# Kernel optimization log

Measured on AMD Instinct MI355X. Metric: run time of the kernel, lower is better.

Reference implementation:

```python
import jax, jax.numpy as jnp
import numpy as np

H = 256      # input_size == hidden_size
N = 512      # x dim0: acts as LSTM time axis (torch unbatched 2D LSTM input)
S = 128      # x dim1: independent seq positions (outer python loop in torch)
UP = 4       # upscale


def setup_inputs() -> dict:
    key = jax.random.key(0)
    ks = jax.random.split(key, 9)
    k_init = 1.0 / np.sqrt(H)
    u = lambda k, shape: jax.random.uniform(k, shape, jnp.float32, -k_init, k_init)
    return {
        "x": jax.random.normal(ks[0], (N, S, H), jnp.float32),
        # PyTorch nn.LSTM params, gate order (i, f, g, o)
        "Wih0": u(ks[1], (4 * H, H)), "Whh0": u(ks[2], (4 * H, H)),
        "bih0": u(ks[3], (4 * H,)),   "bhh0": u(ks[4], (4 * H,)),
        "Wih1": u(ks[5], (4 * H, H)), "Whh1": u(ks[6], (4 * H, H)),
        "bih1": u(ks[7], (4 * H,)),   "bhh1": u(ks[8], (4 * H,)),
    }


def _lstm_layer(x, h0, c0, Wih, Whh, b):
    """Scan one LSTM layer over the time axis. x: [N, S, H], h0/c0: [S, H]."""
    def step(carry, xt):
        h, c = carry
        g = xt @ Wih.T + h @ Whh.T + b            # [S, 4H]
        i, f, gg, o = jnp.split(g, 4, axis=-1)
        i = jax.nn.sigmoid(i)
        f = jax.nn.sigmoid(f)
        gg = jnp.tanh(gg)
        o = jax.nn.sigmoid(o)
        c = f * c + i * gg
        h = o * jnp.tanh(c)
        return (h, c), h
    (hT, cT), ys = jax.lax.scan(step, (h0, c0), x)
    return ys, hT, cT


def reference(x, Wih0, Whh0, bih0, bhh0, Wih1, Whh1, bih1, bhh1):
    n, s, hdim = x.shape
    # state per seq position (torch's outer loop is vectorized as batch S)
    h = jnp.zeros((2, s, hdim), x.dtype)
    c = jnp.zeros((2, s, hdim), x.dtype)
    b0 = bih0 + bhh0
    b1 = bih1 + bhh1
    data = [x]
    cur = x
    for _ in range(UP - 1):
        y0, h0n, c0n = _lstm_layer(cur, h[0], c[0], Wih0, Whh0, b0)
        y1, h1n, c1n = _lstm_layer(y0, h[1], c[1], Wih1, Whh1, b1)
        h = jnp.stack([h0n, h1n])
        c = jnp.stack([c0n, c1n])
        cur = y1
        data.append(y1)
    # torch interleaves per seq position: [..., s*UP + k, ...] = data[k][:, s, :]
    out = jnp.stack(data, axis=2)          # [N, S, UP, H]
    return out.reshape(n, s * UP, hdim)
```

## Files before the change

### kernel.cpp

```cpp
#include <hip/hip_runtime.h>
#include <stdint.h>

#define Hh 256
#define Sd 128
#define Nt 512
#define NPASS 3
#define TSTEPS (NPASS*Nt)
#define RBLK 16
#define POIS 0x7F80u
#define LEAD 192

typedef float f32x4 __attribute__((ext_vector_type(4)));
typedef __bf16 bf16x8 __attribute__((ext_vector_type(8)));
typedef unsigned short u16x8 __attribute__((ext_vector_type(8)));
typedef unsigned long long ull;
typedef ull ull2 __attribute__((ext_vector_type(2)));

#define HBUF_ELEMS ((size_t)Nt*Sd*Hh)
#define WPACK_OFF  (2ull*HBUF_ELEMS*2)
#define FLAGS_OFF  (WPACK_OFF + 2097152ull)

__device__ __forceinline__ unsigned short f2bf(float f) {
  unsigned u = __builtin_bit_cast(unsigned, f);
  u += 0x7FFFu + ((u >> 16) & 1u);
  return (unsigned short)(u >> 16);
}
__device__ __forceinline__ ull pk4(float a, float b, float c, float d) {
  return (ull)f2bf(a) | ((ull)f2bf(b) << 16) | ((ull)f2bf(c) << 32) | ((ull)f2bf(d) << 48);
}
__device__ __forceinline__ bool hasPois(ull v) {
  return ((unsigned short)(v)       == (unsigned short)POIS) |
         ((unsigned short)(v >> 16) == (unsigned short)POIS) |
         ((unsigned short)(v >> 32) == (unsigned short)POIS) |
         ((unsigned short)(v >> 48) == (unsigned short)POIS);
}
__device__ __forceinline__ ull ld8(const void* p) {
  return __hip_atomic_load((ull*)p, __ATOMIC_RELAXED, __HIP_MEMORY_SCOPE_AGENT);
}
__device__ __forceinline__ void st8c(void* p, ull v) {
  __hip_atomic_store((ull*)p, v, __ATOMIC_RELAXED, __HIP_MEMORY_SCOPE_AGENT);
}
__device__ __forceinline__ void poll2(const ull* p, ull& a0, ull& a1) {
  while (hasPois(a0) | hasPois(a1)) {
    __builtin_amdgcn_s_sleep(1);
    if (hasPois(a0)) a0 = ld8(p);
    if (hasPois(a1)) a1 = ld8(p + 1);
  }
}
__device__ __forceinline__ void bar_lgkm() {
  __builtin_amdgcn_sched_barrier(0);
  asm volatile("s_waitcnt lgkmcnt(0)" ::: "memory");
  __builtin_amdgcn_s_barrier();
  __builtin_amdgcn_sched_barrier(0);
}

__global__ void pack_w(const float* __restrict__ Wih0, const float* __restrict__ Whh0,
                       const float* __restrict__ Wih1, const float* __restrict__ Whh1,
                       unsigned short* __restrict__ wpack) {
  int id = blockIdx.x * 256 + threadIdx.x;
  int ln = id & 63;
  int kt = (id >> 6) & 15;
  int w  = (id >> 10) & 7;
  int g2 = (id >> 13) & 7;
  int l  = (id >> 16) & 1;
  int col = (w >> 1)*256 + g2*32 + (w & 1)*16 + (ln & 15);
  int k0 = kt*32 + (ln >> 4)*8;
  const float* Wih = l ? Wih1 : Wih0;
  const float* Whh = l ? Whh1 : Whh0;
  const float* src = (k0 < 256) ? (Wih + (size_t)col*256 + k0)
                                : (Whh + (size_t)col*256 + (k0 - 256));
  u16x8 v;
#pragma unroll
  for (int j = 0; j < 8; ++j) v[j] = f2bf(src[j]);
  *(u16x8*)(wpack + (size_t)id * 8) = v;
}

__global__ void copy_x(const float* __restrict__ x, float* __restrict__ out) {
  int id = blockIdx.x * 256 + threadIdx.x;
  int n  = id >> 13;
  int s  = (id >> 6) & 127;
  int h4 = id & 63;
  const float4 v = *(const float4*)(x + ((size_t)n*Sd + s)*Hh + h4*4);
  *(float4*)(out + ((size_t)n*(Sd*4) + s*4)*Hh + h4*4) = v;
}

__global__ void poison_hbuf(unsigned int* __restrict__ p) {
  size_t i = (size_t)blockIdx.x * 256 + threadIdx.x;
  uint4 v = make_uint4(0x7F807F80u, 0x7F807F80u, 0x7F807F80u, 0x7F807F80u);
  *(uint4*)(p + i*4) = v;
}

__global__ void __launch_bounds__(512) lstm_persist(
    const float* __restrict__ x,
    const float* __restrict__ bih0, const float* __restrict__ bhh0,
    const float* __restrict__ bih1, const float* __restrict__ bhh1,
    const unsigned short* __restrict__ wpack,
    unsigned short* __restrict__ hbuf,
    unsigned int* __restrict__ prog,
    float* __restrict__ out)
{
  const int b = blockIdx.x;
  const int r = b & 7;
  const int g2 = (b >> 3) & 7;
  const int l = (b >> 6) & 1;
  const int tid = threadIdx.x;
  const int ln = tid & 63;
  const int w  = tid >> 6;

  __shared__ __align__(16) unsigned short AinB[2][RBLK * 256];
  __shared__ __align__(16) unsigned short Ah[RBLK * 256];
  __shared__ float gates[RBLK][132];

  bf16x8 B[16];
  {
    const unsigned short* base = wpack + ((size_t)((l*8 + g2)*8 + w)) * 8192 + (size_t)ln * 8;
#pragma unroll
    for (int kt = 0; kt < 16; ++kt) {
      u16x8 u = *(const u16x8*)(base + kt * 512);
      B[kt] = __builtin_bit_cast(bf16x8, u);
    }
  }

  const int srow = tid >> 5;
  const int cc   = tid & 31;
  const int s    = r*RBLK + srow;
  const int hcol = g2*32 + cc;
  float bias[4];
  {
    const float* bi = l ? bih1 : bih0;
    const float* bh = l ? bhh1 : bhh0;
#pragma unroll
    for (int q = 0; q < 4; ++q) {
      int col = q*256 + g2*32 + cc;
      bias[q] = bi[col] + bh[col];
    }
  }
  float cst = 0.f;

  const int row_f = ln & 15;
  const int kg16  = (ln >> 4) * 16;
  const int swr   = (row_f & 7) << 4;
  const int stAddr = srow*512 + ((cc*16) ^ ((srow & 7) << 4));

  unsigned int* flagL1 = prog + r*8;
  unsigned int* myFlag = prog + r*8 + g2;
  const unsigned short* hbufL0 = hbuf;
  unsigned short* hbufSelf = hbuf + (size_t)l * HBUF_ELEMS;

  float4 pxa, pxb;
  ull pa = 0, pb = 0;
  ull hpa = 0, hpb = 0;

  auto writeAin = [&](int buf, ull lo, ull hi) {
    ull2 v = {lo, hi};
    *(ull2*)((char*)AinB[buf] + stAddr) = v;
  };
  auto prefetchAin = [&](int T2) {
    const int t2 = T2 & 511, p2 = T2 >> 9;
    if (l == 1) {
      const ull* ip = (const ull*)(hbufL0 + ((size_t)t2*Sd + s)*Hh + cc*8);
      pa = ld8(ip); pb = ld8(ip + 1);
    } else if (p2 == 0) {
      const float* xb = x + ((size_t)t2*Sd + s)*Hh + cc*8;
      pxa = *(const float4*)(xb);
      pxb = *(const float4*)(xb + 4);
    } else {
      const float* ob = out + ((size_t)t2*(Sd*4) + s*4 + p2)*Hh + cc*8;
      pxa = *(const float4*)(ob);
      pxb = *(const float4*)(ob + 4);
    }
  };
  auto consumeAin = [&](int T1) {
    const int buf = T1 & 1;
    if (l == 1) {
      if (hasPois(pa) | hasPois(pb)) {
        const int t1 = T1 & 511;
        const ull* ip = (const ull*)(hbufL0 + ((size_t)t1*Sd + s)*Hh + cc*8);
        poll2(ip, pa, pb);
      }
      writeAin(buf, pa, pb);
    } else {
      writeAin(buf, pk4(pxa.x, pxa.y, pxa.z, pxa.w), pk4(pxb.x, pxb.y, pxb.z, pxb.w));
    }
  };

#define MFMA4(BUF, BOFF)                                                            \
  {                                                                                 \
    _Pragma("unroll")                                                               \
    for (int kt = 0; kt < 8; kt += 2) {                                             \
      int off0 = row_f*512 + (( kt     *64 + kg16) ^ swr);                          \
      int off1 = row_f*512 + (((kt + 1)*64 + kg16) ^ swr);                          \
      u16x8 a0 = *(const u16x8*)((const char*)(BUF) + off0);                        \
      u16x8 a1 = *(const u16x8*)((const char*)(BUF) + off1);                        \
      acc0 = __builtin_amdgcn_mfma_f32_16x16x32_bf16(                               \
               __builtin_bit_cast(bf16x8, a0), B[BOFF + kt],     acc0, 0,0,0);      \
      acc1 = __builtin_amdgcn_mfma_f32_16x16x32_bf16(                               \
               __builtin_bit_cast(bf16x8, a1), B[BOFF + kt + 1], acc1, 0,0,0);      \
    }                                                                               \
  }

  f32x4 acc0 = {0.f,0.f,0.f,0.f}, acc1 = {0.f,0.f,0.f,0.f};
  if (l == 1) {
    const ull* ip = (const ull*)(hbufL0 + (size_t)s*Hh + cc*8);
    ull a0 = ld8(ip), a1 = ld8(ip + 1);
    poll2(ip, a0, a1);
    writeAin(0, a0, a1);
  } else {
    const float* xb = x + (size_t)s*Hh + cc*8;
    float4 v0 = *(const float4*)(xb), v1 = *(const float4*)(xb + 4);
    writeAin(0, pk4(v0.x, v0.y, v0.z, v0.w), pk4(v1.x, v1.y, v1.z, v1.w));
  }
  prefetchAin(1);
  __syncthreads();
  MFMA4(AinB[0], 0)

  for (int T = 0; T < TSTEPS; ++T) {
    const int p = T >> 9;
    const int t = T & 511;

    if (T > 0) {
      const ull* ap = (const ull*)(hbufSelf + ((size_t)((T - 1) & 511)*Sd + s)*Hh + cc*8);
      ull a0 = hpa, a1 = hpb;
      while (hasPois(a0) | hasPois(a1)) {
        if (hasPois(a0)) a0 = ld8(ap);
        if (hasPois(a1)) a1 = ld8(ap + 1);
      }
      ull2 v2 = {a0, a1};
      *(ull2*)((char*)Ah + stAddr) = v2;
    } else {
      ull2 v2 = {0ull, 0ull};
      *(ull2*)((char*)Ah + stAddr) = v2;
    }
    if (T + 1 < TSTEPS) consumeAin(T + 1);
    if (l == 0 && (T & 15) == 0 && tid < 8) {
      int need = T - LEAD;
      if (need > 0)
        while ((int)__hip_atomic_load(flagL1 + tid, __ATOMIC_RELAXED, __HIP_MEMORY_SCOPE_AGENT) < need)
          __builtin_amdgcn_s_sleep(1);
    }
    bar_lgkm();

    if (T > 0) MFMA4(Ah, 8)

    {
      const int colb = (w >> 1)*32 + (w & 1)*16 + (ln & 15);
      const int rowb = (ln >> 4)*4;
#pragma unroll
      for (int j = 0; j < 4; ++j)
        gates[rowb + j][colb] = acc0[j] + acc1[j];
    }
    bar_lgkm();

    {
      float G0 = gates[srow][cc]      + bias[0];
      float G1 = gates[srow][32 + cc] + bias[1];
      float G2 = gates[srow][64 + cc] + bias[2];
      float G3 = gates[srow][96 + cc] + bias[3];
      float gi = 1.f/(1.f + __expf(-G0));
      float gf = 1.f/(1.f + __expf(-G1));
      float gg = 1.f - 2.f/(1.f + __expf(2.f*G2));
      float go = 1.f/(1.f + __expf(-G3));
      cst = gf*cst + gi*gg;
      float th = 1.f - 2.f/(1.f + __expf(2.f*cst));
      float hv = go*th;
      float h1 = __shfl_down(hv, 1);
      float h2 = __shfl_down(hv, 2);
      float h3 = __shfl_down(hv, 3);
      if ((cc & 3) == 0) {
        st8c(hbufSelf + ((size_t)t*Sd + s)*Hh + hcol, pk4(hv, h1, h2, h3));
        st8c(hbufSelf + ((size_t)((T + 256) & 511)*Sd + s)*Hh + hcol,
             0x7F807F807F807F80ull);
      }
      if (l == 1 && (cc & 1) == 0) {
        ull o01 = ((ull)__builtin_bit_cast(unsigned, hv))
                | ((ull)__builtin_bit_cast(unsigned, h1) << 32);
        st8c(out + ((size_t)t*(Sd*4) + s*4 + (p + 1))*Hh + hcol, o01);
      }
    }
    if (l == 1 && (T & 15) == 15 && tid == 0)
      __hip_atomic_store(myFlag, (unsigned)(T + 1), __ATOMIC_RELAXED, __HIP_MEMORY_SCOPE_AGENT);
    if (T + 2 < TSTEPS) prefetchAin(T + 2);
    if (T + 1 < TSTEPS) {
      const ull* ap = (const ull*)(hbufSelf + ((size_t)(T & 511)*Sd + s)*Hh + cc*8);
      hpa = ld8(ap);
      hpb = ld8(ap + 1);
    }
    acc0 = (f32x4){0.f,0.f,0.f,0.f};
    acc1 = (f32x4){0.f,0.f,0.f,0.f};
    if (T + 1 < TSTEPS) MFMA4(AinB[(T + 1) & 1], 0)
  }
}

extern "C" void kernel_launch(void* const* d_in, const int* in_sizes, int n_in,
                              void* d_out, int out_size, void* d_ws, size_t ws_size,
                              hipStream_t stream) {
  const float* x    = (const float*)d_in[0];
  const float* Wih0 = (const float*)d_in[1];
  const float* Whh0 = (const float*)d_in[2];
  const float* bih0 = (const float*)d_in[3];
  const float* bhh0 = (const float*)d_in[4];
  const float* Wih1 = (const float*)d_in[5];
  const float* Whh1 = (const float*)d_in[6];
  const float* bih1 = (const float*)d_in[7];
  const float* bhh1 = (const float*)d_in[8];
  float* out = (float*)d_out;
  char* ws = (char*)d_ws;

  if (ws_size < FLAGS_OFF + 4096) return;

  unsigned short* hbuf  = (unsigned short*)ws;
  unsigned short* wpack = (unsigned short*)(ws + WPACK_OFF);
  unsigned int*   prog  = (unsigned int*)(ws + FLAGS_OFF);

  (void)hipMemsetAsync(prog, 0, 1024, stream);
  hipLaunchKernelGGL(poison_hbuf, dim3(16384), dim3(256), 0, stream, (unsigned int*)hbuf);
  hipLaunchKernelGGL(pack_w, dim3(512), dim3(256), 0, stream, Wih0, Whh0, Wih1, Whh1, wpack);
  hipLaunchKernelGGL(copy_x, dim3(16384), dim3(256), 0, stream, x, out);
  hipLaunchKernelGGL(lstm_persist, dim3(128), dim3(512), 0, stream,
                     x, bih0, bhh0, bih1, bhh1, wpack, hbuf, prog, out);
}
```

Baseline: 3.185 ms.

## Process two row blocks per workgroup and halve the persistent grid

Each persistent workgroup now handles two 16-row batch chunks instead of one, so the grid shrinks from 128 to 64 blocks while the per-block weight registers are reused across both chunks. The two chunks' MFMA, gate math and global loads are interleaved, which hides latency within a step and reduces the number of cross-block participants in the recurrent dependency chain. The cost is double the per-step work on each block's critical path, more LDS and registers, and only half the CUs in use.

After: 5.681 ms. +78.3%, slower.

```diff
diff --git a/kernel.cpp b/kernel.cpp
--- a/kernel.cpp
+++ b/kernel.cpp
@@ -100,16 +100,16 @@
     float* __restrict__ out)
 {
   const int b = blockIdx.x;
-  const int r = b & 7;
-  const int g2 = (b >> 3) & 7;
-  const int l = (b >> 6) & 1;
+  const int rgp = b & 3;
+  const int g2 = (b >> 2) & 7;
+  const int l = (b >> 5) & 1;
   const int tid = threadIdx.x;
   const int ln = tid & 63;
   const int w  = tid >> 6;
 
-  __shared__ __align__(16) unsigned short AinB[2][RBLK * 256];
-  __shared__ __align__(16) unsigned short Ah[RBLK * 256];
-  __shared__ float gates[RBLK][132];
+  __shared__ __align__(16) unsigned short AinB[2][2][RBLK * 256];
+  __shared__ __align__(16) unsigned short Ah[2][RBLK * 256];
+  __shared__ float gates[2][RBLK][132];
 
   bf16x8 B[16];
   {
@@ -123,8 +123,10 @@
 
   const int srow = tid >> 5;
   const int cc   = tid & 31;
-  const int s    = r*RBLK + srow;
   const int hcol = g2*32 + cc;
+  int sC[2];
+  sC[0] = (rgp*2    )*RBLK + srow;
+  sC[1] = (rgp*2 + 1)*RBLK + srow;
   float bias[4];
   {
     const float* bi = l ? bih1 : bih0;
@@ -135,56 +137,21 @@
       bias[q] = bi[col] + bh[col];
     }
   }
-  float cst = 0.f;
+  float cst[2] = {0.f, 0.f};
 
   const int row_f = ln & 15;
   const int kg16  = (ln >> 4) * 16;
   const int swr   = (row_f & 7) << 4;
   const int stAddr = srow*512 + ((cc*16) ^ ((srow & 7) << 4));
 
-  unsigned int* flagL1 = prog + r*8;
-  unsigned int* myFlag = prog + r*8 + g2;
   const unsigned short* hbufL0 = hbuf;
   unsigned short* hbufSelf = hbuf + (size_t)l * HBUF_ELEMS;
 
-  float4 pxa, pxb;
-  ull pa = 0, pb = 0;
-  ull hpa = 0, hpb = 0;
-
-  auto writeAin = [&](int buf, ull lo, ull hi) {
-    ull2 v = {lo, hi};
-    *(ull2*)((char*)AinB[buf] + stAddr) = v;
-  };
-  auto prefetchAin = [&](int T2) {
-    const int t2 = T2 & 511, p2 = T2 >> 9;
-    if (l == 1) {
-      const ull* ip = (const ull*)(hbufL0 + ((size_t)t2*Sd + s)*Hh + cc*8);
-      pa = ld8(ip); pb = ld8(ip + 1);
-    } else if (p2 == 0) {
-      const float* xb = x + ((size_t)t2*Sd + s)*Hh + cc*8;
-      pxa = *(const float4*)(xb);
-      pxb = *(const float4*)(xb + 4);
-    } else {
-      const float* ob = out + ((size_t)t2*(Sd*4) + s*4 + p2)*Hh + cc*8;
-      pxa = *(const float4*)(ob);
-      pxb = *(const float4*)(ob + 4);
-    }
-  };
-  auto consumeAin = [&](int T1) {
-    const int buf = T1 & 1;
-    if (l == 1) {
-      if (hasPois(pa) | hasPois(pb)) {
-        const int t1 = T1 & 511;
-        const ull* ip = (const ull*)(hbufL0 + ((size_t)t1*Sd + s)*Hh + cc*8);
-        poll2(ip, pa, pb);
-      }
-      writeAin(buf, pa, pb);
-    } else {
-      writeAin(buf, pk4(pxa.x, pxa.y, pxa.z, pxa.w), pk4(pxb.x, pxb.y, pxb.z, pxb.w));
-    }
-  };
-
-#define MFMA4(BUF, BOFF)                                                            \
+  float4 pxa[2], pxb[2];
+  ull pa[2] = {0,0}, pb[2] = {0,0};
+  ull hpa[2] = {0,0}, hpb[2] = {0,0};
+
+#define MFMA4(BUF, BOFF, A0, A1)                                                    \
   {                                                                                 \
     _Pragma("unroll")                                                               \
     for (int kt = 0; kt < 8; kt += 2) {                                             \
@@ -192,102 +159,169 @@
       int off1 = row_f*512 + (((kt + 1)*64 + kg16) ^ swr);                          \
       u16x8 a0 = *(const u16x8*)((const char*)(BUF) + off0);                        \
       u16x8 a1 = *(const u16x8*)((const char*)(BUF) + off1);                        \
-      acc0 = __builtin_amdgcn_mfma_f32_16x16x32_bf16(                               \
-               __builtin_bit_cast(bf16x8, a0), B[BOFF + kt],     acc0, 0,0,0);      \
-      acc1 = __builtin_amdgcn_mfma_f32_16x16x32_bf16(                               \
-               __builtin_bit_cast(bf16x8, a1), B[BOFF + kt + 1], acc1, 0,0,0);      \
+      A0 = __builtin_amdgcn_mfma_f32_16x16x32_bf16(                                 \
+               __builtin_bit_cast(bf16x8, a0), B[BOFF + kt],     A0, 0,0,0);        \
+      A1 = __builtin_amdgcn_mfma_f32_16x16x32_bf16(                                 \
+               __builtin_bit_cast(bf16x8, a1), B[BOFF + kt + 1], A1, 0,0,0);        \
     }                                                                               \
   }
 
-  f32x4 acc0 = {0.f,0.f,0.f,0.f}, acc1 = {0.f,0.f,0.f,0.f};
-  if (l == 1) {
-    const ull* ip = (const ull*)(hbufL0 + (size_t)s*Hh + cc*8);
-    ull a0 = ld8(ip), a1 = ld8(ip + 1);
-    poll2(ip, a0, a1);
-    writeAin(0, a0, a1);
-  } else {
-    const float* xb = x + (size_t)s*Hh + cc*8;
-    float4 v0 = *(const float4*)(xb), v1 = *(const float4*)(xb + 4);
-    writeAin(0, pk4(v0.x, v0.y, v0.z, v0.w), pk4(v1.x, v1.y, v1.z, v1.w));
-  }
-  prefetchAin(1);
+  f32x4 acc0[2], acc1[2];
+
+#pragma unroll
+  for (int c = 0; c < 2; ++c) {
+    if (l == 1) {
+      const ull* ip = (const ull*)(hbufL0 + (size_t)sC[c]*Hh + cc*8);
+      ull a0 = ld8(ip), a1 = ld8(ip + 1);
+      poll2(ip, a0, a1);
+      ull2 v = {a0, a1}; *(ull2*)((char*)AinB[c][0] + stAddr) = v;
+    } else {
+      const float* xb = x + (size_t)sC[c]*Hh + cc*8;
+      float4 v0 = *(const float4*)(xb), v1 = *(const float4*)(xb + 4);
+      ull2 v = {pk4(v0.x, v0.y, v0.z, v0.w), pk4(v1.x, v1.y, v1.z, v1.w)};
+      *(ull2*)((char*)AinB[c][0] + stAddr) = v;
+    }
+    if (l == 1) {
+      const ull* ip = (const ull*)(hbufL0 + ((size_t)1*Sd + sC[c])*Hh + cc*8);
+      pa[c] = ld8(ip); pb[c] = ld8(ip + 1);
+    } else {
+      const float* xb = x + ((size_t)1*Sd + sC[c])*Hh + cc*8;
+      pxa[c] = *(const float4*)(xb);
+      pxb[c] = *(const float4*)(xb + 4);
+    }
+  }
   __syncthreads();
-  MFMA4(AinB[0], 0)
+#pragma unroll
+  for (int c = 0; c < 2; ++c) {
+    acc0[c] = (f32x4){0.f,0.f,0.f,0.f};
+    acc1[c] = (f32x4){0.f,0.f,0.f,0.f};
+    MFMA4(AinB[c][0], 0, acc0[c], acc1[c])
+  }
 
   for (int T = 0; T < TSTEPS; ++T) {
     const int p = T >> 9;
     const int t = T & 511;
 
-    if (T > 0) {
-      const ull* ap = (const ull*)(hbufSelf + ((size_t)((T - 1) & 511)*Sd + s)*Hh + cc*8);
-      ull a0 = hpa, a1 = hpb;
-      while (hasPois(a0) | hasPois(a1)) {
-        if (hasPois(a0)) a0 = ld8(ap);
-        if (hasPois(a1)) a1 = ld8(ap + 1);
-      }
-      ull2 v2 = {a0, a1};
-      *(ull2*)((char*)Ah + stAddr) = v2;
-    } else {
-      ull2 v2 = {0ull, 0ull};
-      *(ull2*)((char*)Ah + stAddr) = v2;
-    }
-    if (T + 1 < TSTEPS) consumeAin(T + 1);
-    if (l == 0 && (T & 15) == 0 && tid < 8) {
+#pragma unroll
+    for (int c = 0; c < 2; ++c) {
+      if (T > 0) {
+        const ull* ap = (const ull*)(hbufSelf + ((size_t)((T - 1) & 511)*Sd + sC[c])*Hh + cc*8);
+        ull a0 = hpa[c], a1 = hpb[c];
+        while (hasPois(a0) | hasPois(a1)) {
+          if (hasPois(a0)) a0 = ld8(ap);
+          if (hasPois(a1)) a1 = ld8(ap + 1);
+        }
+        ull2 v2 = {a0, a1};
+        *(ull2*)((char*)Ah[c] + stAddr) = v2;
+      } else {
+        ull2 v2 = {0ull, 0ull};
+        *(ull2*)((char*)Ah[c] + stAddr) = v2;
+      }
+    }
+    if (T + 1 < TSTEPS) {
+#pragma unroll
+      for (int c = 0; c < 2; ++c) {
+        const int buf = (T + 1) & 1;
+        if (l == 1) {
+          ull a0 = pa[c], a1 = pb[c];
+          if (hasPois(a0) | hasPois(a1)) {
+            const ull* ip = (const ull*)(hbufL0 + ((size_t)((T + 1) & 511)*Sd + sC[c])*Hh + cc*8);
+            poll2(ip, a0, a1);
+          }
+          ull2 v = {a0, a1}; *(ull2*)((char*)AinB[c][buf] + stAddr) = v;
+        } else {
+          ull2 v = {pk4(pxa[c].x, pxa[c].y, pxa[c].z, pxa[c].w),
+                    pk4(pxb[c].x, pxb[c].y, pxb[c].z, pxb[c].w)};
+          *(ull2*)((char*)AinB[c][buf] + stAddr) = v;
+        }
+      }
+    }
+    if (l == 0 && (T & 15) == 0 && tid < 16) {
       int need = T - LEAD;
-      if (need > 0)
-        while ((int)__hip_atomic_load(flagL1 + tid, __ATOMIC_RELAXED, __HIP_MEMORY_SCOPE_AGENT) < need)
+      if (need > 0) {
+        unsigned int* fl = prog + (rgp*2 + (tid >> 3))*8 + (tid & 7);
+        while ((int)__hip_atomic_load(fl, __ATOMIC_RELAXED, __HIP_MEMORY_SCOPE_AGENT) < need)
           __builtin_amdgcn_s_sleep(1);
+      }
     }
     bar_lgkm();
-
-    if (T > 0) MFMA4(Ah, 8)
 
     {
       const int colb = (w >> 1)*32 + (w & 1)*16 + (ln & 15);
       const int rowb = (ln >> 4)*4;
 #pragma unroll
-      for (int j = 0; j < 4; ++j)
-        gates[rowb + j][colb] = acc0[j] + acc1[j];
+      for (int c = 0; c < 2; ++c) {
+        if (T > 0) MFMA4(Ah[c], 8, acc0[c], acc1[c])
+#pragma unroll
+        for (int j = 0; j < 4; ++j)
+          gates[c][rowb + j][colb] = acc0[c][j] + acc1[c][j];
+      }
     }
     bar_lgkm();
 
-    {
-      float G0 = gates[srow][cc]      + bias[0];
-      float G1 = gates[srow][32 + cc] + bias[1];
-      float G2 = gates[srow][64 + cc] + bias[2];
-      float G3 = gates[srow][96 + cc] + bias[3];
+#pragma unroll
+    for (int c = 0; c < 2; ++c) {
+      float G0 = gates[c][srow][cc]      + bias[0];
+      float G1 = gates[c][srow][32 + cc] + bias[1];
+      float G2 = gates[c][srow][64 + cc] + bias[2];
+      float G3 = gates[c][srow][96 + cc] + bias[3];
       float gi = 1.f/(1.f + __expf(-G0));
       float gf = 1.f/(1.f + __expf(-G1));
       float gg = 1.f - 2.f/(1.f + __expf(2.f*G2));
       float go = 1.f/(1.f + __expf(-G3));
-      cst = gf*cst + gi*gg;
-      float th = 1.f - 2.f/(1.f + __expf(2.f*cst));
+      cst[c] = gf*cst[c] + gi*gg;
+      float th = 1.f - 2.f/(1.f + __expf(2.f*cst[c]));
       float hv = go*th;
       float h1 = __shfl_down(hv, 1);
       float h2 = __shfl_down(hv, 2);
       float h3 = __shfl_down(hv, 3);
       if ((cc & 3) == 0) {
-        st8c(hbufSelf + ((size_t)t*Sd + s)*Hh + hcol, pk4(hv, h1, h2, h3));
-        st8c(hbufSelf + ((size_t)((T + 256) & 511)*Sd + s)*Hh + hcol,
+        st8c(hbufSelf + ((size_t)t*Sd + sC[c])*Hh + hcol, pk4(hv, h1, h2, h3));
+        st8c(hbufSelf + ((size_t)((T + 256) & 511)*Sd + sC[c])*Hh + hcol,
              0x7F807F807F807F80ull);
       }
       if (l == 1 && (cc & 1) == 0) {
         ull o01 = ((ull)__builtin_bit_cast(unsigned, hv))
                 | ((ull)__builtin_bit_cast(unsigned, h1) << 32);
-        st8c(out + ((size_t)t*(Sd*4) + s*4 + (p + 1))*Hh + hcol, o01);
-      }
-    }
-    if (l == 1 && (T & 15) == 15 && tid == 0)
-      __hip_atomic_store(myFlag, (unsigned)(T + 1), __ATOMIC_RELAXED, __HIP_MEMORY_SCOPE_AGENT);
-    if (T + 2 < TSTEPS) prefetchAin(T + 2);
-    if (T + 1 < TSTEPS) {
-      const ull* ap = (const ull*)(hbufSelf + ((size_t)(T & 511)*Sd + s)*Hh + cc*8);
-      hpa = ld8(ap);
-      hpb = ld8(ap + 1);
-    }
-    acc0 = (f32x4){0.f,0.f,0.f,0.f};
-    acc1 = (f32x4){0.f,0.f,0.f,0.f};
-    if (T + 1 < TSTEPS) MFMA4(AinB[(T + 1) & 1], 0)
+        st8c(out + ((size_t)t*(Sd*4) + sC[c]*4 + (p + 1))*Hh + hcol, o01);
+      }
+    }
+    if (l == 1 && (T & 15) == 15 && tid == 0) {
+      __hip_atomic_store(prog + (rgp*2    )*8 + g2, (unsigned)(T + 1),
+                         __ATOMIC_RELAXED, __HIP_MEMORY_SCOPE_AGENT);
+      __hip_atomic_store(prog + (rgp*2 + 1)*8 + g2, (unsigned)(T + 1),
+                         __ATOMIC_RELAXED, __HIP_MEMORY_SCOPE_AGENT);
+    }
+
+#pragma unroll
+    for (int c = 0; c < 2; ++c) {
+      if (T + 2 < TSTEPS) {
+        const int t2 = (T + 2) & 511, p2 = (T + 2) >> 9;
+        if (l == 1) {
+          const ull* ip = (const ull*)(hbufL0 + ((size_t)t2*Sd + sC[c])*Hh + cc*8);
+          pa[c] = ld8(ip); pb[c] = ld8(ip + 1);
+        } else if (p2 == 0) {
+          const float* xb = x + ((size_t)t2*Sd + sC[c])*Hh + cc*8;
+          pxa[c] = *(const float4*)(xb);
+          pxb[c] = *(const float4*)(xb + 4);
+        } else {
+          const float* ob = out + ((size_t)t2*(Sd*4) + sC[c]*4 + p2)*Hh + cc*8;
+          pxa[c] = *(const float4*)(ob);
+          pxb[c] = *(const float4*)(ob + 4);
+        }
+      }
+      if (T + 1 < TSTEPS) {
+        const ull* ap = (const ull*)(hbufSelf + ((size_t)(T & 511)*Sd + sC[c])*Hh + cc*8);
+        hpa[c] = ld8(ap);
+        hpb[c] = ld8(ap + 1);
+      }
+    }
+#pragma unroll
+    for (int c = 0; c < 2; ++c) {
+      acc0[c] = (f32x4){0.f,0.f,0.f,0.f};
+      acc1[c] = (f32x4){0.f,0.f,0.f,0.f};
+      if (T + 1 < TSTEPS) MFMA4(AinB[c][(T + 1) & 1], 0, acc0[c], acc1[c])
+    }
   }
 }
 
@@ -316,6 +350,6 @@
   hipLaunchKernelGGL(poison_hbuf, dim3(16384), dim3(256), 0, stream, (unsigned int*)hbuf);
   hipLaunchKernelGGL(pack_w, dim3(512), dim3(256), 0, stream, Wih0, Whh0, Wih1, Whh1, wpack);
   hipLaunchKernelGGL(copy_x, dim3(16384), dim3(256), 0, stream, x, out);
-  hipLaunchKernelGGL(lstm_persist, dim3(128), dim3(512), 0, stream,
+  hipLaunchKernelGGL(lstm_persist, dim3(64), dim3(512), 0, stream,
                      x, bih0, bhh0, bih1, bhh1, wpack, hbuf, prog, out);
 }
```

## Halve block size and give each wave two weight tiles and two hidden units

Applied to the files above, without the earlier changes.

The persistent LSTM kernel now runs 256 threads per block instead of 512. Each wave holds two B-fragment sets and issues four MFMAs per k-step, sharing each A-fragment load across two tiles. Each thread computes the gate nonlinearities for two hidden columns and moves twice the data per load and store. This cuts barrier participants and LDS A-reads per step, at the cost of higher register pressure and longer serial per-thread work on the recurrent critical path.

Result: slower. 3.826 ms (+20.1%).

```diff
diff --git a/kernel.cpp b/kernel.cpp
--- a/kernel.cpp
+++ b/kernel.cpp
@@ -40,11 +40,13 @@
 __device__ __forceinline__ void st8c(void* p, ull v) {
   __hip_atomic_store((ull*)p, v, __ATOMIC_RELAXED, __HIP_MEMORY_SCOPE_AGENT);
 }
-__device__ __forceinline__ void poll2(const ull* p, ull& a0, ull& a1) {
-  while (hasPois(a0) | hasPois(a1)) {
-    __builtin_amdgcn_s_sleep(1);
-    if (hasPois(a0)) a0 = ld8(p);
-    if (hasPois(a1)) a1 = ld8(p + 1);
+__device__ __forceinline__ void poll4(const ull* p, ull a[4]) {
+  for (;;) {
+    bool st = hasPois(a[0]) | hasPois(a[1]) | hasPois(a[2]) | hasPois(a[3]);
+    if (!st) return;
+#pragma unroll
+    for (int u = 0; u < 4; ++u)
+      if (hasPois(a[u])) a[u] = ld8(p + u);
   }
 }
 __device__ __forceinline__ void bar_lgkm() {
@@ -90,7 +92,7 @@
   *(uint4*)(p + i*4) = v;
 }
 
-__global__ void __launch_bounds__(512) lstm_persist(
+__global__ void __launch_bounds__(256, 1) lstm_persist(
     const float* __restrict__ x,
     const float* __restrict__ bih0, const float* __restrict__ bhh0,
     const float* __restrict__ bih1, const float* __restrict__ bhh1,
@@ -111,80 +113,93 @@
   __shared__ __align__(16) unsigned short Ah[RBLK * 256];
   __shared__ float gates[RBLK][132];
 
-  bf16x8 B[16];
+  bf16x8 B0[16], B1[16];
   {
-    const unsigned short* base = wpack + ((size_t)((l*8 + g2)*8 + w)) * 8192 + (size_t)ln * 8;
+    const unsigned short* base0 = wpack + ((size_t)((l*8 + g2)*8 + 2*w    )) * 8192 + (size_t)ln * 8;
+    const unsigned short* base1 = wpack + ((size_t)((l*8 + g2)*8 + 2*w + 1)) * 8192 + (size_t)ln * 8;
 #pragma unroll
     for (int kt = 0; kt < 16; ++kt) {
-      u16x8 u = *(const u16x8*)(base + kt * 512);
-      B[kt] = __builtin_bit_cast(bf16x8, u);
-    }
-  }
-
-  const int srow = tid >> 5;
-  const int cc   = tid & 31;
+      u16x8 u0 = *(const u16x8*)(base0 + kt * 512);
+      u16x8 u1 = *(const u16x8*)(base1 + kt * 512);
+      B0[kt] = __builtin_bit_cast(bf16x8, u0);
+      B1[kt] = __builtin_bit_cast(bf16x8, u1);
+    }
+  }
+
+  const int srow = tid >> 4;
+  const int cp   = tid & 15;
   const int s    = r*RBLK + srow;
-  const int hcol = g2*32 + cc;
-  float bias[4];
+  const int hc0  = cp;
+  const int hcol0 = g2*32 + cp;
+  float bias0[4], bias1[4];
   {
     const float* bi = l ? bih1 : bih0;
     const float* bh = l ? bhh1 : bhh0;
 #pragma unroll
     for (int q = 0; q < 4; ++q) {
-      int col = q*256 + g2*32 + cc;
-      bias[q] = bi[col] + bh[col];
-    }
-  }
-  float cst = 0.f;
+      int col = q*256 + g2*32 + cp;
+      bias0[q] = bi[col] + bh[col];
+      bias1[q] = bi[col + 16] + bh[col + 16];
+    }
+  }
+  float cst0 = 0.f, cst1 = 0.f;
 
   const int row_f = ln & 15;
   const int kg16  = (ln >> 4) * 16;
   const int swr   = (row_f & 7) << 4;
-  const int stAddr = srow*512 + ((cc*16) ^ ((srow & 7) << 4));
+  const int sw    = (srow & 7) << 4;
+  const int stAddr0 = srow*512 + ((cp*32)      ^ sw);
+  const int stAddr1 = srow*512 + ((cp*32 + 16) ^ sw);
 
   unsigned int* flagL1 = prog + r*8;
   unsigned int* myFlag = prog + r*8 + g2;
   const unsigned short* hbufL0 = hbuf;
   unsigned short* hbufSelf = hbuf + (size_t)l * HBUF_ELEMS;
 
-  float4 pxa, pxb;
-  ull pa = 0, pb = 0;
-  ull hpa = 0, hpb = 0;
-
-  auto writeAin = [&](int buf, ull lo, ull hi) {
-    ull2 v = {lo, hi};
-    *(ull2*)((char*)AinB[buf] + stAddr) = v;
+  float4 px[4];
+  ull pa[4] = {0,0,0,0};
+  ull hp[4] = {0,0,0,0};
+
+  auto writeAin = [&](int buf, ull v0, ull v1, ull v2, ull v3) {
+    ull2 a = {v0, v1}; *(ull2*)((char*)AinB[buf] + stAddr0) = a;
+    ull2 c = {v2, v3}; *(ull2*)((char*)AinB[buf] + stAddr1) = c;
   };
   auto prefetchAin = [&](int T2) {
     const int t2 = T2 & 511, p2 = T2 >> 9;
     if (l == 1) {
-      const ull* ip = (const ull*)(hbufL0 + ((size_t)t2*Sd + s)*Hh + cc*8);
-      pa = ld8(ip); pb = ld8(ip + 1);
+      const ull* ip = (const ull*)(hbufL0 + ((size_t)t2*Sd + s)*Hh + cp*16);
+#pragma unroll
+      for (int u = 0; u < 4; ++u) pa[u] = ld8(ip + u);
     } else if (p2 == 0) {
-      const float* xb = x + ((size_t)t2*Sd + s)*Hh + cc*8;
-      pxa = *(const float4*)(xb);
-      pxb = *(const float4*)(xb + 4);
+      const float* xb = x + ((size_t)t2*Sd + s)*Hh + cp*16;
+#pragma unroll
+      for (int u = 0; u < 4; ++u) px[u] = *(const float4*)(xb + 4*u);
     } else {
-      const float* ob = out + ((size_t)t2*(Sd*4) + s*4 + p2)*Hh + cc*8;
-      pxa = *(const float4*)(ob);
-      pxb = *(const float4*)(ob + 4);
+      const float* ob = out + ((size_t)t2*(Sd*4) + s*4 + p2)*Hh + cp*16;
+#pragma unroll
+      for (int u = 0; u < 4; ++u) px[u] = *(const float4*)(ob + 4*u);
     }
   };
   auto consumeAin = [&](int T1) {
     const int buf = T1 & 1;
     if (l == 1) {
-      if (hasPois(pa) | hasPois(pb)) {
-        const int t1 = T1 & 511;
-        const ull* ip = (const ull*)(hbufL0 + ((size_t)t1*Sd + s)*Hh + cc*8);
-        poll2(ip, pa, pb);
-      }
-      writeAin(buf, pa, pb);
+      if (hasPois(pa[0]) | hasPois(pa[1]) | hasPois(pa[2]) | hasPois(pa[3])) {
+        const ull* ip = (const ull*)(hbufL0 + ((size_t)(T1 & 511)*Sd + s)*Hh + cp*16);
+        poll4(ip, pa);
+      }
+      writeAin(buf, pa[0], pa[1], pa[2], pa[3]);
     } else {
-      writeAin(buf, pk4(pxa.x, pxa.y, pxa.z, pxa.w), pk4(pxb.x, pxb.y, pxb.z, pxb.w));
+      writeAin(buf,
+               pk4(px[0].x, px[0].y, px[0].z, px[0].w),
+               pk4(px[1].x, px[1].y, px[1].z, px[1].w),
+               pk4(px[2].x, px[2].y, px[2].z, px[2].w),
+               pk4(px[3].x, px[3].y, px[3].z, px[3].w));
     }
   };
 
-#define MFMA4(BUF, BOFF)                                                            \
+  f32x4 acc00, acc01, acc10, acc11;
+
+#define MFMA8(BUF, BOFF)                                                            \
   {                                                                                 \
     _Pragma("unroll")                                                               \
     for (int kt = 0; kt < 8; kt += 2) {                                             \
@@ -192,44 +207,47 @@
       int off1 = row_f*512 + (((kt + 1)*64 + kg16) ^ swr);                          \
       u16x8 a0 = *(const u16x8*)((const char*)(BUF) + off0);                        \
       u16x8 a1 = *(const u16x8*)((const char*)(BUF) + off1);                        \
-      acc0 = __builtin_amdgcn_mfma_f32_16x16x32_bf16(                               \
-               __builtin_bit_cast(bf16x8, a0), B[BOFF + kt],     acc0, 0,0,0);      \
-      acc1 = __builtin_amdgcn_mfma_f32_16x16x32_bf16(                               \
-               __builtin_bit_cast(bf16x8, a1), B[BOFF + kt + 1], acc1, 0,0,0);      \
+      bf16x8 af0 = __builtin_bit_cast(bf16x8, a0);                                  \
+      bf16x8 af1 = __builtin_bit_cast(bf16x8, a1);                                  \
+      acc00 = __builtin_amdgcn_mfma_f32_16x16x32_bf16(af0, B0[BOFF + kt],     acc00, 0,0,0); \
+      acc10 = __builtin_amdgcn_mfma_f32_16x16x32_bf16(af0, B1[BOFF + kt],     acc10, 0,0,0); \
+      acc01 = __builtin_amdgcn_mfma_f32_16x16x32_bf16(af1, B0[BOFF + kt + 1], acc01, 0,0,0); \
+      acc11 = __builtin_amdgcn_mfma_f32_16x16x32_bf16(af1, B1[BOFF + kt + 1], acc11, 0,0,0); \
     }                                                                               \
   }
 
-  f32x4 acc0 = {0.f,0.f,0.f,0.f}, acc1 = {0.f,0.f,0.f,0.f};
+  acc00 = acc01 = acc10 = acc11 = (f32x4){0.f,0.f,0.f,0.f};
   if (l == 1) {
-    const ull* ip = (const ull*)(hbufL0 + (size_t)s*Hh + cc*8);
-    ull a0 = ld8(ip), a1 = ld8(ip + 1);
-    poll2(ip, a0, a1);
-    writeAin(0, a0, a1);
+    const ull* ip = (const ull*)(hbufL0 + (size_t)s*Hh + cp*16);
+    ull a[4];
+#pragma unroll
+    for (int u = 0; u < 4; ++u) a[u] = ld8(ip + u);
+    poll4(ip, a);
+    writeAin(0, a[0], a[1], a[2], a[3]);
   } else {
-    const float* xb = x + (size_t)s*Hh + cc*8;
-    float4 v0 = *(const float4*)(xb), v1 = *(const float4*)(xb + 4);
-    writeAin(0, pk4(v0.x, v0.y, v0.z, v0.w), pk4(v1.x, v1.y, v1.z, v1.w));
+    const float* xb = x + (size_t)s*Hh + cp*16;
+    float4 v0 = *(const float4*)(xb),     v1 = *(const float4*)(xb + 4);
+    float4 v2 = *(const float4*)(xb + 8), v3 = *(const float4*)(xb + 12);
+    writeAin(0, pk4(v0.x, v0.y, v0.z, v0.w), pk4(v1.x, v1.y, v1.z, v1.w),
+                pk4(v2.x, v2.y, v2.z, v2.w), pk4(v3.x, v3.y, v3.z, v3.w));
   }
   prefetchAin(1);
   __syncthreads();
-  MFMA4(AinB[0], 0)
+  MFMA8(AinB[0], 0)
 
   for (int T = 0; T < TSTEPS; ++T) {
     const int p = T >> 9;
     const int t = T & 511;
 
     if (T > 0) {
-      const ull* ap = (const ull*)(hbufSelf + ((size_t)((T - 1) & 511)*Sd + s)*Hh + cc*8);
-      ull a0 = hpa, a1 = hpb;
-      while (hasPois(a0) | hasPois(a1)) {
-        if (hasPois(a0)) a0 = ld8(ap);
-        if (hasPois(a1)) a1 = ld8(ap + 1);
-      }
-      ull2 v2 = {a0, a1};
-      *(ull2*)((char*)Ah + stAddr) = v2;
+      const ull* ap = (const ull*)(hbufSelf + ((size_t)((T - 1) & 511)*Sd + s)*Hh + cp*16);
+      poll4(ap, hp);
+      ull2 v0 = {hp[0], hp[1]}; *(ull2*)((char*)Ah + stAddr0) = v0;
+      ull2 v1 = {hp[2], hp[3]}; *(ull2*)((char*)Ah + stAddr1) = v1;
     } else {
-      ull2 v2 = {0ull, 0ull};
-      *(ull2*)((char*)Ah + stAddr) = v2;
+      ull2 z = {0ull, 0ull};
+      *(ull2*)((char*)Ah + stAddr0) = z;
+      *(ull2*)((char*)Ah + stAddr1) = z;
     }
     if (T + 1 < TSTEPS) consumeAin(T + 1);
     if (l == 0 && (T & 15) == 0 && tid < 8) {
@@ -240,54 +258,75 @@
     }
     bar_lgkm();
 
-    if (T > 0) MFMA4(Ah, 8)
+    if (T > 0) MFMA8(Ah, 8)
 
     {
-      const int colb = (w >> 1)*32 + (w & 1)*16 + (ln & 15);
+      const int colb = w*32 + (ln & 15);
       const int rowb = (ln >> 4)*4;
 #pragma unroll
-      for (int j = 0; j < 4; ++j)
-        gates[rowb + j][colb] = acc0[j] + acc1[j];
+      for (int j = 0; j < 4; ++j) {
+        gates[rowb + j][colb]      = acc00[j] + acc01[j];
+        gates[rowb + j][colb + 16] = acc10[j] + acc11[j];
+      }
     }
     bar_lgkm();
 
     {
-      float G0 = gates[srow][cc]      + bias[0];
-      float G1 = gates[srow][32 + cc] + bias[1];
-      float G2 = gates[srow][64 + cc] + bias[2];
-      float G3 = gates[srow][96 + cc] + bias[3];
-      float gi = 1.f/(1.f + __expf(-G0));
-      float gf = 1.f/(1.f + __expf(-G1));
-      float gg = 1.f - 2.f/(1.f + __expf(2.f*G2));
-      float go = 1.f/(1.f + __expf(-G3));
-      cst = gf*cst + gi*gg;
-      float th = 1.f - 2.f/(1.f + __expf(2.f*cst));
-      float hv = go*th;
-      float h1 = __shfl_down(hv, 1);
-      float h2 = __shfl_down(hv, 2);
-      float h3 = __shfl_down(hv, 3);
-      if ((cc & 3) == 0) {
-        st8c(hbufSelf + ((size_t)t*Sd + s)*Hh + hcol, pk4(hv, h1, h2, h3));
-        st8c(hbufSelf + ((size_t)((T + 256) & 511)*Sd + s)*Hh + hcol,
-             0x7F807F807F807F80ull);
-      }
-      if (l == 1 && (cc & 1) == 0) {
-        ull o01 = ((ull)__builtin_bit_cast(unsigned, hv))
-                | ((ull)__builtin_bit_cast(unsigned, h1) << 32);
-        st8c(out + ((size_t)t*(Sd*4) + s*4 + (p + 1))*Hh + hcol, o01);
+      float hv0, hv1;
+      {
+        float G0 = gates[srow][hc0]      + bias0[0];
+        float G1 = gates[srow][32 + hc0] + bias0[1];
+        float G2 = gates[srow][64 + hc0] + bias0[2];
+        float G3 = gates[srow][96 + hc0] + bias0[3];
+        float gi = 1.f/(1.f + __expf(-G0));
+        float gf = 1.f/(1.f + __expf(-G1));
+        float gg = 1.f - 2.f/(1.f + __expf(2.f*G2));
+        float go = 1.f/(1.f + __expf(-G3));
+        cst0 = gf*cst0 + gi*gg;
+        hv0 = go*(1.f - 2.f/(1.f + __expf(2.f*cst0)));
+      }
+      {
+        float G0 = gates[srow][16 + hc0]  + bias1[0];
+        float G1 = gates[srow][48 + hc0]  + bias1[1];
+        float G2 = gates[srow][80 + hc0]  + bias1[2];
+        float G3 = gates[srow][112 + hc0] + bias1[3];
+        float gi = 1.f/(1.f + __expf(-G0));
+        float gf = 1.f/(1.f + __expf(-G1));
+        float gg = 1.f - 2.f/(1.f + __expf(2.f*G2));
+        float go = 1.f/(1.f + __expf(-G3));
+        cst1 = gf*cst1 + gi*gg;
+        hv1 = go*(1.f - 2.f/(1.f + __expf(2.f*cst1)));
+      }
+      float a1 = __shfl_down(hv0, 1), a2 = __shfl_down(hv0, 2), a3 = __shfl_down(hv0, 3);
+      float b1 = __shfl_down(hv1, 1), b2 = __shfl_down(hv1, 2), b3 = __shfl_down(hv1, 3);
+      if ((cp & 3) == 0) {
+        unsigned short* hb = hbufSelf + ((size_t)t*Sd + s)*Hh + hcol0;
+        unsigned short* pb = hbufSelf + ((size_t)((T + 256) & 511)*Sd + s)*Hh + hcol0;
+        st8c(hb,      pk4(hv0, a1, a2, a3));
+        st8c(hb + 16, pk4(hv1, b1, b2, b3));
+        st8c(pb,      0x7F807F807F807F80ull);
+        st8c(pb + 16, 0x7F807F807F807F80ull);
+      }
+      if (l == 1 && (cp & 1) == 0) {
+        float* ob = out + ((size_t)t*(Sd*4) + s*4 + (p + 1))*Hh + hcol0;
+        ull o0 = ((ull)__builtin_bit_cast(unsigned, hv0))
+               | ((ull)__builtin_bit_cast(unsigned, a1) << 32);
+        ull o1 = ((ull)__builtin_bit_cast(unsigned, hv1))
+               | ((ull)__builtin_bit_cast(unsigned, b1) << 32);
+        st8c(ob,      o0);
+        st8c(ob + 16, o1);
       }
     }
     if (l == 1 && (T & 15) == 15 && tid == 0)
       __hip_atomic_store(myFlag, (unsigned)(T + 1), __ATOMIC_RELAXED, __HIP_MEMORY_SCOPE_AGENT);
     if (T + 2 < TSTEPS) prefetchAin(T + 2);
     if (T + 1 < TSTEPS) {
-      const ull* ap = (const ull*)(hbufSelf + ((size_t)(T & 511)*Sd + s)*Hh + cc*8);
-      hpa = ld8(ap);
-      hpb = ld8(ap + 1);
-    }
-    acc0 = (f32x4){0.f,0.f,0.f,0.f};
-    acc1 = (f32x4){0.f,0.f,0.f,0.f};
-    if (T + 1 < TSTEPS) MFMA4(AinB[(T + 1) & 1], 0)
+      const ull* ap = (const ull*)(hbufSelf + ((size_t)(T & 511)*Sd + s)*Hh + cp*16);
+#pragma unroll
+      for (int u = 0; u < 4; ++u) hp[u] = ld8(ap + u);
+    }
+    acc00 = acc01 = acc10 = acc11 = (f32x4){0.f,0.f,0.f,0.f};
+    if (T + 1 < TSTEPS) MFMA8(AinB[(T + 1) & 1], 0)
   }
 }
 
@@ -316,6 +355,6 @@
   hipLaunchKernelGGL(poison_hbuf, dim3(16384), dim3(256), 0, stream, (unsigned int*)hbuf);
   hipLaunchKernelGGL(pack_w, dim3(512), dim3(256), 0, stream, Wih0, Whh0, Wih1, Whh1, wpack);
   hipLaunchKernelGGL(copy_x, dim3(16384), dim3(256), 0, stream, x, out);
-  hipLaunchKernelGGL(lstm_persist, dim3(128), dim3(512), 0, stream,
+  hipLaunchKernelGGL(lstm_persist, dim3(128), dim3(256), 0, stream,
                      x, bih0, bhh0, bih1, bhh1, wpack, hbuf, prog, out);
 }
```

## Halve persistent grid by giving each block two hidden-column groups

Applied to the files above, without the earlier changes.

The persistent LSTM kernel now runs 64 blocks instead of 128, and each block covers 64 hidden columns (two former column groups) for its row block. Each wave holds two sets of weight fragments in registers and issues twice as many MFMAs per A-fragment load. Gate staging and the activation math are widened to match, and the cross-layer flag array shrinks to 4 per row group. The aim is to reuse each A-fragment LDS read across two weight sets and to cut the number of blocks that signal and poll each other. The cost is double the per-step compute on the serial recurrence path and higher register pressure (launch bounds now request 2 blocks per CU).

After: 4.204 ms. +32.0%, slower.

```diff
diff --git a/kernel.cpp b/kernel.cpp
--- a/kernel.cpp
+++ b/kernel.cpp
@@ -90,7 +90,7 @@
   *(uint4*)(p + i*4) = v;
 }
 
-__global__ void __launch_bounds__(512) lstm_persist(
+__global__ void __launch_bounds__(512, 2) lstm_persist(
     const float* __restrict__ x,
     const float* __restrict__ bih0, const float* __restrict__ bhh0,
     const float* __restrict__ bih1, const float* __restrict__ bhh1,
@@ -100,50 +100,54 @@
     float* __restrict__ out)
 {
   const int b = blockIdx.x;
-  const int r = b & 7;
-  const int g2 = (b >> 3) & 7;
-  const int l = (b >> 6) & 1;
+  const int g = b & 3;
+  const int r = (b >> 2) & 7;
+  const int l = (b >> 5) & 1;
   const int tid = threadIdx.x;
   const int ln = tid & 63;
   const int w  = tid >> 6;
 
   __shared__ __align__(16) unsigned short AinB[2][RBLK * 256];
   __shared__ __align__(16) unsigned short Ah[RBLK * 256];
-  __shared__ float gates[RBLK][132];
-
-  bf16x8 B[16];
+  __shared__ float gates[RBLK][260];
+
+  bf16x8 B0[16], B1[16];
   {
-    const unsigned short* base = wpack + ((size_t)((l*8 + g2)*8 + w)) * 8192 + (size_t)ln * 8;
+    const unsigned short* base0 =
+      wpack + ((size_t)((l*8 + (g*2 + (w & 1)))*8 + (w >> 1)*2)) * 8192 + (size_t)ln * 8;
 #pragma unroll
     for (int kt = 0; kt < 16; ++kt) {
-      u16x8 u = *(const u16x8*)(base + kt * 512);
-      B[kt] = __builtin_bit_cast(bf16x8, u);
+      u16x8 u0 = *(const u16x8*)(base0 + kt * 512);
+      u16x8 u1 = *(const u16x8*)(base0 + 8192 + kt * 512);
+      B0[kt] = __builtin_bit_cast(bf16x8, u0);
+      B1[kt] = __builtin_bit_cast(bf16x8, u1);
     }
   }
 
   const int srow = tid >> 5;
   const int cc   = tid & 31;
   const int s    = r*RBLK + srow;
-  const int hcol = g2*32 + cc;
-  float bias[4];
+  const int hcol0 = g*64 + cc;
+  float bias0[4], bias1[4];
   {
     const float* bi = l ? bih1 : bih0;
     const float* bh = l ? bhh1 : bhh0;
 #pragma unroll
     for (int q = 0; q < 4; ++q) {
-      int col = q*256 + g2*32 + cc;
-      bias[q] = bi[col] + bh[col];
-    }
-  }
-  float cst = 0.f;
+      int col = q*256 + g*64 + cc;
+      bias0[q] = bi[col] + bh[col];
+      bias1[q] = bi[col + 32] + bh[col + 32];
+    }
+  }
+  float cst0 = 0.f, cst1 = 0.f;
 
   const int row_f = ln & 15;
   const int kg16  = (ln >> 4) * 16;
   const int swr   = (row_f & 7) << 4;
   const int stAddr = srow*512 + ((cc*16) ^ ((srow & 7) << 4));
 
-  unsigned int* flagL1 = prog + r*8;
-  unsigned int* myFlag = prog + r*8 + g2;
+  unsigned int* flagL1 = prog + r*4;
+  unsigned int* myFlag = prog + r*4 + g;
   const unsigned short* hbufL0 = hbuf;
   unsigned short* hbufSelf = hbuf + (size_t)l * HBUF_ELEMS;
 
@@ -174,8 +178,7 @@
     const int buf = T1 & 1;
     if (l == 1) {
       if (hasPois(pa) | hasPois(pb)) {
-        const int t1 = T1 & 511;
-        const ull* ip = (const ull*)(hbufL0 + ((size_t)t1*Sd + s)*Hh + cc*8);
+        const ull* ip = (const ull*)(hbufL0 + ((size_t)(T1 & 511)*Sd + s)*Hh + cc*8);
         poll2(ip, pa, pb);
       }
       writeAin(buf, pa, pb);
@@ -184,7 +187,9 @@
     }
   };
 
-#define MFMA4(BUF, BOFF)                                                            \
+  f32x4 acc00, acc01, acc10, acc11;
+
+#define MFMA8(BUF, BOFF)                                                            \
   {                                                                                 \
     _Pragma("unroll")                                                               \
     for (int kt = 0; kt < 8; kt += 2) {                                             \
@@ -192,14 +197,16 @@
       int off1 = row_f*512 + (((kt + 1)*64 + kg16) ^ swr);                          \
       u16x8 a0 = *(const u16x8*)((const char*)(BUF) + off0);                        \
       u16x8 a1 = *(const u16x8*)((const char*)(BUF) + off1);                        \
-      acc0 = __builtin_amdgcn_mfma_f32_16x16x32_bf16(                               \
-               __builtin_bit_cast(bf16x8, a0), B[BOFF + kt],     acc0, 0,0,0);      \
-      acc1 = __builtin_amdgcn_mfma_f32_16x16x32_bf16(                               \
-               __builtin_bit_cast(bf16x8, a1), B[BOFF + kt + 1], acc1, 0,0,0);      \
+      bf16x8 af0 = __builtin_bit_cast(bf16x8, a0);                                  \
+      bf16x8 af1 = __builtin_bit_cast(bf16x8, a1);                                  \
+      acc00 = __builtin_amdgcn_mfma_f32_16x16x32_bf16(af0, B0[BOFF + kt],     acc00, 0,0,0); \
+      acc10 = __builtin_amdgcn_mfma_f32_16x16x32_bf16(af0, B1[BOFF + kt],     acc10, 0,0,0); \
+      acc01 = __builtin_amdgcn_mfma_f32_16x16x32_bf16(af1, B0[BOFF + kt + 1], acc01, 0,0,0); \
+      acc11 = __builtin_amdgcn_mfma_f32_16x16x32_bf16(af1, B1[BOFF + kt + 1], acc11, 0,0,0); \
     }                                                                               \
   }
 
-  f32x4 acc0 = {0.f,0.f,0.f,0.f}, acc1 = {0.f,0.f,0.f,0.f};
+  acc00 = acc01 = acc10 = acc11 = (f32x4){0.f,0.f,0.f,0.f};
   if (l == 1) {
     const ull* ip = (const ull*)(hbufL0 + (size_t)s*Hh + cc*8);
     ull a0 = ld8(ip), a1 = ld8(ip + 1);
@@ -212,7 +219,7 @@
   }
   prefetchAin(1);
   __syncthreads();
-  MFMA4(AinB[0], 0)
+  MFMA8(AinB[0], 0)
 
   for (int T = 0; T < TSTEPS; ++T) {
     const int p = T >> 9;
@@ -232,7 +239,7 @@
       *(ull2*)((char*)Ah + stAddr) = v2;
     }
     if (T + 1 < TSTEPS) consumeAin(T + 1);
-    if (l == 0 && (T & 15) == 0 && tid < 8) {
+    if (l == 0 && (T & 15) == 0 && tid < 4) {
       int need = T - LEAD;
       if (need > 0)
         while ((int)__hip_atomic_load(flagL1 + tid, __ATOMIC_RELAXED, __HIP_MEMORY_SCOPE_AGENT) < need)
@@ -240,41 +247,63 @@
     }
     bar_lgkm();
 
-    if (T > 0) MFMA4(Ah, 8)
+    if (T > 0) MFMA8(Ah, 8)
 
     {
-      const int colb = (w >> 1)*32 + (w & 1)*16 + (ln & 15);
+      const int colb = w*32 + (ln & 15);
       const int rowb = (ln >> 4)*4;
 #pragma unroll
-      for (int j = 0; j < 4; ++j)
-        gates[rowb + j][colb] = acc0[j] + acc1[j];
+      for (int j = 0; j < 4; ++j) {
+        gates[rowb + j][colb]      = acc00[j] + acc01[j];
+        gates[rowb + j][colb + 16] = acc10[j] + acc11[j];
+      }
     }
     bar_lgkm();
 
     {
-      float G0 = gates[srow][cc]      + bias[0];
-      float G1 = gates[srow][32 + cc] + bias[1];
-      float G2 = gates[srow][64 + cc] + bias[2];
-      float G3 = gates[srow][96 + cc] + bias[3];
-      float gi = 1.f/(1.f + __expf(-G0));
-      float gf = 1.f/(1.f + __expf(-G1));
-      float gg = 1.f - 2.f/(1.f + __expf(2.f*G2));
-      float go = 1.f/(1.f + __expf(-G3));
-      cst = gf*cst + gi*gg;
-      float th = 1.f - 2.f/(1.f + __expf(2.f*cst));
-      float hv = go*th;
-      float h1 = __shfl_down(hv, 1);
-      float h2 = __shfl_down(hv, 2);
-      float h3 = __shfl_down(hv, 3);
+      float hv0, hv1;
+      {
+        float G0 = gates[srow][cc]        + bias0[0];
+        float G1 = gates[srow][64 + cc]   + bias0[1];
+        float G2 = gates[srow][128 + cc]  + bias0[2];
+        float G3 = gates[srow][192 + cc]  + bias0[3];
+        float gi = 1.f/(1.f + __expf(-G0));
+        float gf = 1.f/(1.f + __expf(-G1));
+        float gg = 1.f - 2.f/(1.f + __expf(2.f*G2));
+        float go = 1.f/(1.f + __expf(-G3));
+        cst0 = gf*cst0 + gi*gg;
+        hv0 = go*(1.f - 2.f/(1.f + __expf(2.f*cst0)));
+      }
+      {
+        float G0 = gates[srow][32 + cc]   + bias1[0];
+        float G1 = gates[srow][96 + cc]   + bias1[1];
+        float G2 = gates[srow][160 + cc]  + bias1[2];
+        float G3 = gates[srow][224 + cc]  + bias1[3];
+        float gi = 1.f/(1.f + __expf(-G0));
+        float gf = 1.f/(1.f + __expf(-G1));
+        float gg = 1.f - 2.f/(1.f + __expf(2.f*G2));
+        float go = 1.f/(1.f + __expf(-G3));
+        cst1 = gf*cst1 + gi*gg;
+        hv1 = go*(1.f - 2.f/(1.f + __expf(2.f*cst1)));
+      }
+      float a1 = __shfl_down(hv0, 1), a2 = __shfl_down(hv0, 2), a3 = __shfl_down(hv0, 3);
+      float b1 = __shfl_down(hv1, 1), b2 = __shfl_down(hv1, 2), b3 = __shfl_down(hv1, 3);
       if ((cc & 3) == 0) {
-        st8c(hbufSelf + ((size_t)t*Sd + s)*Hh + hcol, pk4(hv, h1, h2, h3));
-        st8c(hbufSelf + ((size_t)((T + 256) & 511)*Sd + s)*Hh + hcol,
-             0x7F807F807F807F80ull);
+        unsigned short* hb = hbufSelf + ((size_t)t*Sd + s)*Hh + hcol0;
+        unsigned short* pbz = hbufSelf + ((size_t)((T + 256) & 511)*Sd + s)*Hh + hcol0;
+        st8c(hb,      pk4(hv0, a1, a2, a3));
+        st8c(hb + 32, pk4(hv1, b1, b2, b3));
+        st8c(pbz,      0x7F807F807F807F80ull);
+        st8c(pbz + 32, 0x7F807F807F807F80ull);
       }
       if (l == 1 && (cc & 1) == 0) {
-        ull o01 = ((ull)__builtin_bit_cast(unsigned, hv))
-                | ((ull)__builtin_bit_cast(unsigned, h1) << 32);
-        st8c(out + ((size_t)t*(Sd*4) + s*4 + (p + 1))*Hh + hcol, o01);
+        float* ob = out + ((size_t)t*(Sd*4) + s*4 + (p + 1))*Hh + hcol0;
+        ull o0 = ((ull)__builtin_bit_cast(unsigned, hv0))
+               | ((ull)__builtin_bit_cast(unsigned, a1) << 32);
+        ull o1 = ((ull)__builtin_bit_cast(unsigned, hv1))
+               | ((ull)__builtin_bit_cast(unsigned, b1) << 32);
+        st8c(ob,      o0);
+        st8c(ob + 32, o1);
       }
     }
     if (l == 1 && (T & 15) == 15 && tid == 0)
@@ -285,9 +314,8 @@
       hpa = ld8(ap);
       hpb = ld8(ap + 1);
     }
-    acc0 = (f32x4){0.f,0.f,0.f,0.f};
-    acc1 = (f32x4){0.f,0.f,0.f,0.f};
-    if (T + 1 < TSTEPS) MFMA4(AinB[(T + 1) & 1], 0)
+    acc00 = acc01 = acc10 = acc11 = (f32x4){0.f,0.f,0.f,0.f};
+    if (T + 1 < TSTEPS) MFMA8(AinB[(T + 1) & 1], 0)
   }
 }
 
@@ -316,6 +344,6 @@
   hipLaunchKernelGGL(poison_hbuf, dim3(16384), dim3(256), 0, stream, (unsigned int*)hbuf);
   hipLaunchKernelGGL(pack_w, dim3(512), dim3(256), 0, stream, Wih0, Whh0, Wih1, Whh1, wpack);
   hipLaunchKernelGGL(copy_x, dim3(16384), dim3(256), 0, stream, x, out);
-  hipLaunchKernelGGL(lstm_persist, dim3(128), dim3(512), 0, stream,
+  hipLaunchKernelGGL(lstm_persist, dim3(64), dim3(512), 0, stream,
                      x, bih0, bhh0, bih1, bhh1, wpack, hbuf, prog, out);
 }
```
